# Kernel tuning notes

Hardware: AMD Instinct MI355X
Metric: run time of the kernel (lower is better)

Reference implementation:

```python
import jax, jax.numpy as jnp
import numpy as np

N = 50000   # nodes
E = 800000  # edges
C = 64      # node feature channels (0e)
A = 4       # edge attr channels
B = 16      # edge embedding (radial basis) size
H = 8       # radial MLP hidden size
D = 32      # query/key channels
P = 16      # node attr channels
R_MAX = 5.0


def setup_inputs() -> dict:
    key = jax.random.key(0)
    ks = jax.random.split(key, 20)
    w = lambda k, shape, fan_in: (jax.random.normal(k, shape, jnp.float32) / np.sqrt(fan_in).astype(np.float32))
    inp = {
        "node_feats": jax.random.normal(ks[0], (N, C), jnp.float32),
        "node_attrs": jax.random.normal(ks[1], (N, P), jnp.float32),
        "edge_embedding": jax.random.uniform(ks[2], (E, B), jnp.float32),
        "edge_attrs": jax.random.normal(ks[3], (E, A), jnp.float32),
        "positions": jax.random.normal(ks[4], (N, 3), jnp.float32) * 0.3,  # keep lengths < r_max
        "edge_src": jax.random.randint(ks[5], (E,), 0, N),
        "edge_dst": jax.random.randint(ks[6], (E,), 0, N),
        # parameters
        "W_q": w(ks[7], (C, D), C),            # h_q Linear
        "W1_k": w(ks[8], (B, H), B),           # radial MLP for tp_k
        "W2_k": w(ks[9], (H, C * A), H),
        "W1_v": w(ks[10], (B, H), B),          # radial MLP for tp_v
        "W2_v": w(ks[11], (H, C * A), H),
        "W_lin_k": w(ks[12], (C, D), C),       # linear_k
        "W_lin_v": w(ks[13], (C, C), C),       # linear_v
        "W_dot": w(ks[14], (D, D), D * D),     # FullyConnectedTensorProduct(q,k,'0e')
        "W_sc": w(ks[15], (C, P, C), C * P),   # self connection FCTP
    }
    return inp


def soft_unit_step(x):
    safe = jnp.where(x > 0, x, 1.0)
    return jnp.where(x > 0, jnp.exp(-1.0 / safe), 0.0)


def uvu_tp(x_src, edge_attrs, edge_embedding, W1, W2):
    # radial MLP -> per-edge, per-path weights [E, C, A]; 'uvu' tensor product on scalars
    wgt = (jax.nn.silu(edge_embedding @ W1) @ W2).reshape(-1, C, A)
    return x_src * (jnp.einsum('eca,ea->ec', wgt, edge_attrs) / np.sqrt(A).astype(np.float32))


def reference(node_feats, node_attrs, edge_embedding, edge_attrs, positions,
              edge_src, edge_dst, W_q, W1_k, W2_k, W1_v, W2_v,
              W_lin_k, W_lin_v, W_dot, W_sc):
    q = (node_feats @ W_q)[edge_dst]                              # [E, D]
    x_src = node_feats[edge_src]                                  # [E, C]
    k = uvu_tp(x_src, edge_attrs, edge_embedding, W1_k, W2_k) @ W_lin_k  # [E, D]
    v = uvu_tp(x_src, edge_attrs, edge_embedding, W1_v, W2_v) @ W_lin_v  # [E, C]

    edge_vec = positions[edge_dst] - positions[edge_src]
    edge_length = jnp.linalg.norm(edge_vec, axis=1)               # [E]
    cutoff = soft_unit_step(2.0 * R_MAX * (1.0 - edge_length / R_MAX))

    score = jnp.einsum('ei,ij,ej->e', q, W_dot, k)                # weighted bilinear dot -> 0e
    expv = cutoff * jnp.exp(score)                                # [E]
    z = jax.ops.segment_sum(expv, edge_dst, num_segments=N)       # softmax normalizer
    z = jnp.where(z == 0, 1.0, z)
    alpha = expv / z[edge_dst]
    msg = jnp.sqrt(jax.nn.relu(alpha))[:, None] * v               # [E, C]
    node_out = jax.ops.segment_sum(msg, edge_dst, num_segments=N)  # [N, C]

    sc = jnp.einsum('nc,np,cpo->no', node_feats, node_attrs, W_sc)
    return node_out + sc
```

## Files before the change

kernel.cpp:

```cpp
#include <hip/hip_runtime.h>
#include <math.h>

#define NN 50000
#define EE 800000
#define NPAD 50176

typedef __attribute__((ext_vector_type(8))) short short8v;
typedef __attribute__((ext_vector_type(4))) float f32x4;

static __device__ __forceinline__ short bf16r(float x) {
  union { float f; unsigned u; } v; v.f = x;
  unsigned r = v.u + 0x7FFFu + ((v.u >> 16) & 1u);
  return (short)(r >> 16);
}
static __device__ __forceinline__ float bf2f(unsigned u) {
  union { unsigned u; float f; } v; v.u = u << 16;
  return v.f;
}
static __device__ __forceinline__ unsigned pk2(float a, float b) {
  return (unsigned)(unsigned short)bf16r(a) | ((unsigned)(unsigned short)bf16r(b) << 16);
}


__global__ __launch_bounds__(256) void prep_kernel(
    const float* __restrict__ Wq, const float* __restrict__ Wdot,
    const float* __restrict__ Wlk, const float* __restrict__ W2k,
    const float* __restrict__ W2v, const float* __restrict__ Wlv,
    const float* __restrict__ Wsc, float* __restrict__ M,
    unsigned short* __restrict__ w2kT, unsigned short* __restrict__ w2vT,
    unsigned short* __restrict__ wlvb, unsigned short* __restrict__ wscb,
    int* __restrict__ cur)
{
  const int tid = threadIdx.x;
  const int b = blockIdx.x;
  if (b == 0) {
    __shared__ float tmp[2048];
#pragma unroll
    for (int r = 0; r < 8; ++r) {
      int idx = tid + r * 256;
      int cin = idx >> 5, d = idx & 31;
      float a = 0.f;
      for (int j = 0; j < 32; ++j) a = fmaf(Wq[cin * 32 + j], Wdot[j * 32 + d], a);
      tmp[idx] = a;
    }
    __syncthreads();
#pragma unroll
    for (int r = 0; r < 16; ++r) {
      int idx = tid + r * 256;
      int cin = idx >> 6, c = idx & 63;
      float a = 0.f;
      for (int d = 0; d < 32; ++d) a = fmaf(tmp[cin * 32 + d], Wlk[c * 32 + d], a);
      M[idx] = a;
    }
#pragma unroll
    for (int r = 0; r < 8; ++r) {
      int idx = tid + r * 256;
      int c = idx >> 5, k = idx & 31, h = k >> 2, a = k & 3;
      w2kT[idx] = (unsigned short)bf16r(W2k[h * 256 + c * 4 + a]);
      w2vT[idx] = (unsigned short)bf16r(W2v[h * 256 + c * 4 + a]);
    }
#pragma unroll
    for (int r = 0; r < 16; ++r) {
      int idx = tid + r * 256;
      int o = idx >> 6, c = idx & 63;
      wlvb[idx] = (unsigned short)bf16r(Wlv[c * 64 + o]);
    }
  } else if (b <= 196) {
    cur[(b - 1) * 256 + tid] = 0;
  } else {
    int w = (b - 197) * 256 + tid;
    int c = w & 63, o = (w >> 6) & 63, p = w >> 12;
    wscb[w] = (unsigned short)bf16r(Wsc[c * 1024 + p * 64 + o]);
  }
}

__global__ __launch_bounds__(256) void hist_zero(
    const int* __restrict__ edst, int* __restrict__ cur, float4* __restrict__ zu)
{
  int i = blockIdx.x * 256 + threadIdx.x;
  float4 zf = make_float4(0.f, 0.f, 0.f, 0.f);
  zu[i] = zf;
  if (i < 12544) zu[800000 + i] = zf;
  atomicAdd(&cur[edst[i]], 1);
}

__global__ __launch_bounds__(256) void scanA_kernel(
    int* __restrict__ cur, int* __restrict__ bsum)
{
  __shared__ int s[256];
  const int tid = threadIdx.x;
  const int i = blockIdx.x * 256 + tid;
  int v = cur[i];
  s[tid] = v;
  __syncthreads();
  for (int off = 1; off < 256; off <<= 1) {
    int t = (tid >= off) ? s[tid - off] : 0;
    __syncthreads();
    s[tid] += t;
    __syncthreads();
  }
  cur[i] = s[tid] - v;
  if (tid == 255) bsum[blockIdx.x] = s[255];
}

__global__ __launch_bounds__(256) void scanB_kernel(int* __restrict__ bsum)
{
  __shared__ int s[256];
  const int tid = threadIdx.x;
  int v = (tid < 196) ? bsum[tid] : 0;
  s[tid] = v;
  __syncthreads();
  for (int off = 1; off < 256; off <<= 1) {
    int t = (tid >= off) ? s[tid - off] : 0;
    __syncthreads();
    s[tid] += t;
    __syncthreads();
  }
  if (tid < 196) bsum[tid] = s[tid] - v;
}

__global__ __launch_bounds__(256) void scatter_fused(
    const int* __restrict__ esrc, const int* __restrict__ edst,
    const float* __restrict__ ea, const float* __restrict__ eb,
    const float* __restrict__ pos, const float* __restrict__ W1k,
    const float* __restrict__ W1v, int* __restrict__ cur,
    const int* __restrict__ bsum, int* __restrict__ perm,
    float* __restrict__ rec)
{
  int e = blockIdx.x * 256 + threadIdx.x;
  int s = esrc[e], d = edst[e];
  int r = atomicAdd(&cur[d], 1) + bsum[d >> 8];
  perm[r] = e;
  float dx = pos[d * 3 + 0] - pos[s * 3 + 0];
  float dy = pos[d * 3 + 1] - pos[s * 3 + 1];
  float dz = pos[d * 3 + 2] - pos[s * 3 + 2];
  float len = sqrtf(fmaf(dx, dx, fmaf(dy, dy, dz * dz)));
  float arg = 10.f - 2.f * len;
  float cl = (arg > 0.f) ? __expf(-1.f / arg) : 0.f;
  const f32x4* eb4 = reinterpret_cast<const f32x4*>(eb);
  f32x4 q0 = eb4[e * 4 + 0], q1 = eb4[e * 4 + 1],
        q2 = eb4[e * 4 + 2], q3 = eb4[e * 4 + 3];
  float ebv[16] = {q0.x, q0.y, q0.z, q0.w, q1.x, q1.y, q1.z, q1.w,
                   q2.x, q2.y, q2.z, q2.w, q3.x, q3.y, q3.z, q3.w};
  float h[16];
#pragma unroll
  for (int j = 0; j < 16; ++j) h[j] = 0.f;
#pragma unroll
  for (int b = 0; b < 16; ++b) {
    float x = ebv[b];
#pragma unroll
    for (int j = 0; j < 8; ++j) {
      h[j]     = fmaf(x, W1k[b * 8 + j], h[j]);
      h[8 + j] = fmaf(x, W1v[b * 8 + j], h[8 + j]);
    }
  }
#pragma unroll
  for (int j = 0; j < 16; ++j) h[j] = h[j] / (1.f + __expf(-h[j]));

  f32x4 a4 = reinterpret_cast<const f32x4*>(ea)[e];
  f32x4* rp4 = reinterpret_cast<f32x4*>(rec + (size_t)e * 12);
  f32x4 w0, w1, w2;
  w0.x = cl;
  w0.y = __uint_as_float(pk2(a4.x, a4.y));
  w0.z = __uint_as_float(pk2(a4.z, a4.w));
  w0.w = 0.f;
  w1.x = __uint_as_float(pk2(h[0], h[1]));
  w1.y = __uint_as_float(pk2(h[2], h[3]));
  w1.z = __uint_as_float(pk2(h[4], h[5]));
  w1.w = __uint_as_float(pk2(h[6], h[7]));
  w2.x = __uint_as_float(pk2(h[8], h[9]));
  w2.y = __uint_as_float(pk2(h[10], h[11]));
  w2.z = __uint_as_float(pk2(h[12], h[13]));
  w2.w = __uint_as_float(pk2(h[14], h[15]));
  rp4[0] = w0;
  rp4[1] = w1;
  rp4[2] = w2;
}

__global__ __launch_bounds__(256) void tq_kernel(
    const float* __restrict__ nf, const float* __restrict__ M,
    unsigned short* __restrict__ tqb, unsigned short* __restrict__ nfb)
{
  __shared__ float Ml[4096];
  __shared__ float nfl[64 * 68];
  const int tid = threadIdx.x;
  const int base = blockIdx.x * 64;
#pragma unroll
  for (int r = 0; r < 4; ++r) {
    int idx = tid + r * 256;
    reinterpret_cast<float4*>(Ml)[idx] = reinterpret_cast<const float4*>(M)[idx];
  }
#pragma unroll
  for (int r = 0; r < 4; ++r) {
    int idx = tid + r * 256;
    int row = idx >> 4, c4 = idx & 15;
    float4 v = make_float4(0.f, 0.f, 0.f, 0.f);
    if (base + row < NN) v = reinterpret_cast<const float4*>(nf)[(base + row) * 16 + c4];
    *reinterpret_cast<float4*>(&nfl[row * 68 + c4 * 4]) = v;
  }
  __syncthreads();
  const int to = tid & 15, tn = tid >> 4;
  float4 acc[4] = {make_float4(0,0,0,0), make_float4(0,0,0,0),
                   make_float4(0,0,0,0), make_float4(0,0,0,0)};
  for (int c = 0; c < 64; ++c) {
    float4 m = reinterpret_cast<const float4*>(Ml)[c * 16 + to];
#pragma unroll
    for (int i = 0; i < 4; ++i) {
      float x = nfl[(tn * 4 + i) * 68 + c];
      acc[i].x = fmaf(x, m.x, acc[i].x);
      acc[i].y = fmaf(x, m.y, acc[i].y);
      acc[i].z = fmaf(x, m.z, acc[i].z);
      acc[i].w = fmaf(x, m.w, acc[i].w);
    }
  }
#pragma unroll
  for (int i = 0; i < 4; ++i) {
    int n = base + tn * 4 + i;
    if (n < NN) {
      unsigned* tp = reinterpret_cast<unsigned*>(tqb) + (size_t)n * 32 + to * 2;
      tp[0] = pk2(acc[i].x, acc[i].y);
      tp[1] = pk2(acc[i].z, acc[i].w);
    }
  }
#pragma unroll
  for (int r = 0; r < 8; ++r) {
    int idx = tid + r * 256;
    int row = idx >> 5, cp = idx & 31;
    int n = base + row;
    if (n < NN) {
      reinterpret_cast<unsigned*>(nfb)[(size_t)n * 32 + cp] =
          pk2(nfl[row * 68 + cp * 2], nfl[row * 68 + cp * 2 + 1]);
    }
  }
}

__global__ __launch_bounds__(256) void edge_kernel(
    const unsigned short* __restrict__ nfb, const unsigned short* __restrict__ tqb,
    const float* __restrict__ rec, const int* __restrict__ perm,
    const int* __restrict__ esrc, const int* __restrict__ edst,
    const unsigned short* __restrict__ w2kT, const unsigned short* __restrict__ w2vT,
    float* __restrict__ z, float* __restrict__ U)
{
  __shared__ float xsAll[4][16 * 68];
  __shared__ int   esAll[4][16];
  __shared__ int   edAll[4][16];
  __shared__ float clAll[4][16];
  __shared__ float evAll[4][16];
  const int tid  = threadIdx.x;
  const int lane = tid & 63;
  const int w = tid >> 6;
  const int lo = lane & 15, hi = lane >> 4;
  const int sb = (blockIdx.x * 4 + w) * 16;
  float* xs = xsAll[w];
  int*   es = esAll[w];
  int*   ed = edAll[w];
  float* cl = clAll[w];
  float* evs = evAll[w];

  short8v bk[4], bv[4];
#pragma unroll
  for (int t = 0; t < 4; ++t) {
    bk[t] = *reinterpret_cast<const short8v*>(&w2kT[(16 * t + lo) * 32 + hi * 8]);
    bv[t] = *reinterpret_cast<const short8v*>(&w2vT[(16 * t + lo) * 32 + hi * 8]);
  }

  const int eL = perm[sb + lo];
  const unsigned* ru = reinterpret_cast<const unsigned*>(rec);
  const size_t rb = (size_t)eL * 12;
  unsigned ea01 = ru[rb + 1];
  unsigned ea23 = ru[rb + 2];
  unsigned k01  = ru[rb + 4 + hi];
  unsigned v01  = ru[rb + 8 + hi];
  if (hi == 0) {
    es[lo] = esrc[eL];
    ed[lo] = edst[eL];
    cl[lo] = rec[rb];
  }
  __builtin_amdgcn_wave_barrier();

#pragma unroll
  for (int r = 0; r < 2; ++r) {
    int idx = lane + r * 64;
    int e = idx >> 3, c8 = idx & 7;
    float4 pv = reinterpret_cast<const float4*>(nfb)[(size_t)es[e] * 8 + c8];
    unsigned u0 = __float_as_uint(pv.x), u1 = __float_as_uint(pv.y),
             u2 = __float_as_uint(pv.z), u3 = __float_as_uint(pv.w);
    float* xp = &xs[e * 68 + c8 * 8];
    xp[0] = bf2f(u0 & 0xffffu); xp[1] = bf2f(u0 >> 16);
    xp[2] = bf2f(u1 & 0xffffu); xp[3] = bf2f(u1 >> 16);
    xp[4] = bf2f(u2 & 0xffffu); xp[5] = bf2f(u2 >> 16);
    xp[6] = bf2f(u3 & 0xffffu); xp[7] = bf2f(u3 >> 16);
  }

  float ax = bf2f(ea01 & 0xffffu), ay = bf2f(ea01 >> 16);
  float az = bf2f(ea23 & 0xffffu), aw = bf2f(ea23 >> 16);
  float hk0 = bf2f(k01 & 0xffffu), hk1 = bf2f(k01 >> 16);
  float hv0 = bf2f(v01 & 0xffffu), hv1 = bf2f(v01 >> 16);
  short8v ak, av;
  ak[0] = bf16r(hk0 * ax); ak[1] = bf16r(hk0 * ay);
  ak[2] = bf16r(hk0 * az); ak[3] = bf16r(hk0 * aw);
  ak[4] = bf16r(hk1 * ax); ak[5] = bf16r(hk1 * ay);
  ak[6] = bf16r(hk1 * az); ak[7] = bf16r(hk1 * aw);
  av[0] = bf16r(hv0 * ax); av[1] = bf16r(hv0 * ay);
  av[2] = bf16r(hv0 * az); av[3] = bf16r(hv0 * aw);
  av[4] = bf16r(hv1 * ax); av[5] = bf16r(hv1 * ay);
  av[6] = bf16r(hv1 * az); av[7] = bf16r(hv1 * aw);
  __builtin_amdgcn_wave_barrier();

  f32x4 zero = {0.f, 0.f, 0.f, 0.f};
  f32x4 ack[4], acv[4];
#pragma unroll
  for (int t = 0; t < 4; ++t) {
    ack[t] = __builtin_amdgcn_mfma_f32_16x16x32_bf16(ak, bk[t], zero, 0, 0, 0);
    acv[t] = __builtin_amdgcn_mfma_f32_16x16x32_bf16(av, bv[t], zero, 0, 0, 0);
  }

  const int erow = 4 * hi;
  const unsigned short* tp0 = tqb + (size_t)ed[erow + 0] * 64;
  const unsigned short* tp1 = tqb + (size_t)ed[erow + 1] * 64;
  const unsigned short* tp2 = tqb + (size_t)ed[erow + 2] * 64;
  const unsigned short* tp3 = tqb + (size_t)ed[erow + 3] * 64;
  float p0 = 0.f, p1 = 0.f, p2 = 0.f, p3 = 0.f;
#pragma unroll
  for (int t = 0; t < 4; ++t) {
    int c = lo + 16 * t;
    p0 = fmaf(xs[(erow + 0) * 68 + c] * bf2f(tp0[c]), ack[t][0], p0);
    p1 = fmaf(xs[(erow + 1) * 68 + c] * bf2f(tp1[c]), ack[t][1], p1);
    p2 = fmaf(xs[(erow + 2) * 68 + c] * bf2f(tp2[c]), ack[t][2], p2);
    p3 = fmaf(xs[(erow + 3) * 68 + c] * bf2f(tp3[c]), ack[t][3], p3);
  }
#pragma unroll
  for (int off = 1; off < 16; off <<= 1) {
    p0 += __shfl_xor(p0, off);
    p1 += __shfl_xor(p1, off);
    p2 += __shfl_xor(p2, off);
    p3 += __shfl_xor(p3, off);
  }
  float ev0 = cl[erow + 0] * __expf(0.5f * p0);
  float ev1 = cl[erow + 1] * __expf(0.5f * p1);
  float ev2 = cl[erow + 2] * __expf(0.5f * p2);
  float ev3 = cl[erow + 3] * __expf(0.5f * p3);
  float se0 = sqrtf(ev0), se1 = sqrtf(ev1), se2 = sqrtf(ev2), se3 = sqrtf(ev3);
  if (lo < 4) {
    float ev = (lo == 0) ? ev0 : (lo == 1) ? ev1 : (lo == 2) ? ev2 : ev3;
    evs[erow + lo] = ev;
  }
#pragma unroll
  for (int i = 0; i < 4; ++i) {
    const float se = (i == 0) ? se0 : (i == 1) ? se1 : (i == 2) ? se2 : se3;
    float* xr = &xs[(erow + i) * 68 + lo];
#pragma unroll
    for (int t = 0; t < 4; ++t) {
      xr[16 * t] = se * xr[16 * t] * acv[t][i];
    }
  }
  __builtin_amdgcn_wave_barrier();
  {
    const int c = lane;
    float acc = 0.f, evacc = 0.f;
    int prev = ed[0];
#pragma unroll
    for (int r = 0; r < 16; ++r) {
      int d = ed[r];
      if (d != prev) {
        unsafeAtomicAdd(&U[prev * 64 + c], acc);
        if (c == 0) unsafeAtomicAdd(&z[prev], evacc);
        acc = 0.f; evacc = 0.f; prev = d;
      }
      acc += xs[r * 68 + c];
      if (c == 0) evacc += evs[r];
    }
    unsafeAtomicAdd(&U[prev * 64 + c], acc);
    if (c == 0) unsafeAtomicAdd(&z[prev], evacc);
  }
}

__global__ __launch_bounds__(256, 4) void final_kernel(
    const float* __restrict__ nf, const float* __restrict__ na,
    const float* __restrict__ U, const float* __restrict__ z,
    const unsigned short* __restrict__ wscb, const unsigned short* __restrict__ wlvb,
    float* __restrict__ out)
{
  __shared__ float nfl[64 * 68];
  __shared__ float Ul[64 * 68];
  __shared__ float nal[64 * 17];
  __shared__ float sl[64];
  const int tid = threadIdx.x;
  const int lane = tid & 63;
  const int lo = lane & 15, hi = lane >> 4;
  const int w = tid >> 6;
  const int nb = blockIdx.x * 64;

#pragma unroll
  for (int r = 0; r < 4; ++r) {
    int idx = tid + r * 256;
    int row = idx >> 4, c4 = idx & 15;
    int n = nb + row; if (n >= NN) n = NN - 1;
    float4 v = reinterpret_cast<const float4*>(nf)[n * 16 + c4];
    *reinterpret_cast<float4*>(&nfl[row * 68 + c4 * 4]) = v;
    float4 u = reinterpret_cast<const float4*>(U)[n * 16 + c4];
    *reinterpret_cast<float4*>(&Ul[row * 68 + c4 * 4]) = u;
  }
#pragma unroll
  for (int r = 0; r < 4; ++r) {
    int idx = tid + r * 256;
    int row = idx >> 4, p = idx & 15;
    int n = nb + row; if (n >= NN) n = NN - 1;
    nal[row * 17 + p] = na[n * 16 + p];
  }
  if (tid < 64) {
    int n = nb + tid; if (n >= NN) n = NN - 1;
    float zz = z[n];
    sl[tid] = (zz > 0.f) ? 0.5f * rsqrtf(zz) : 0.f;
  }
  __syncthreads();

  const int row = 16 * w + lo;
  short8v anf[2], au[2];
#pragma unroll
  for (int kk = 0; kk < 2; ++kk) {
#pragma unroll
    for (int j = 0; j < 8; ++j) {
      anf[kk][j] = bf16r(nfl[row * 68 + 32 * kk + 8 * hi + j]);
      au[kk][j]  = bf16r(Ul[row * 68 + 32 * kk + 8 * hi + j]);
    }
  }

  f32x4 zeroA = {0.f, 0.f, 0.f, 0.f};
  f32x4 accS[4] = {zeroA, zeroA, zeroA, zeroA};
  f32x4 accU[4] = {zeroA, zeroA, zeroA, zeroA};

#pragma unroll
  for (int t = 0; t < 4; ++t) {
    short8v b0 = *reinterpret_cast<const short8v*>(&wlvb[(16 * t + lo) * 64 + 8 * hi]);
    short8v b1 = *reinterpret_cast<const short8v*>(&wlvb[(16 * t + lo) * 64 + 32 + 8 * hi]);
    accU[t] = __builtin_amdgcn_mfma_f32_16x16x32_bf16(au[0], b0, accU[t], 0, 0, 0);
    accU[t] = __builtin_amdgcn_mfma_f32_16x16x32_bf16(au[1], b1, accU[t], 0, 0, 0);
  }
#pragma unroll 1
  for (int p = 0; p < 16; ++p) {
    f32x4 cp[4] = {zeroA, zeroA, zeroA, zeroA};
#pragma unroll
    for (int t = 0; t < 4; ++t) {
      const int bbase = (p * 64 + 16 * t + lo) * 64 + 8 * hi;
      short8v b0 = *reinterpret_cast<const short8v*>(&wscb[bbase]);
      short8v b1 = *reinterpret_cast<const short8v*>(&wscb[bbase + 32]);
      cp[t] = __builtin_amdgcn_mfma_f32_16x16x32_bf16(anf[0], b0, cp[t], 0, 0, 0);
      cp[t] = __builtin_amdgcn_mfma_f32_16x16x32_bf16(anf[1], b1, cp[t], 0, 0, 0);
    }
#pragma unroll
    for (int i = 0; i < 4; ++i) {
      float nav = nal[(16 * w + 4 * hi + i) * 17 + p];
#pragma unroll
      for (int t = 0; t < 4; ++t) accS[t][i] = fmaf(nav, cp[t][i], accS[t][i]);
    }
  }
#pragma unroll
  for (int i = 0; i < 4; ++i) {
    int n = nb + 16 * w + 4 * hi + i;
    if (n < NN) {
      float s = sl[16 * w + 4 * hi + i];
#pragma unroll
      for (int t = 0; t < 4; ++t) {
        out[n * 64 + 16 * t + lo] = fmaf(s, accU[t][i], accS[t][i]);
      }
    }
  }
}

extern "C" void kernel_launch(void* const* d_in, const int* in_sizes, int n_in,
                              void* d_out, int out_size, void* d_ws, size_t ws_size,
                              hipStream_t stream) {
  const float* nf   = (const float*)d_in[0];
  const float* na   = (const float*)d_in[1];
  const float* eb   = (const float*)d_in[2];
  const float* ea   = (const float*)d_in[3];
  const float* pos  = (const float*)d_in[4];
  const int*   esrc = (const int*)d_in[5];
  const int*   edst = (const int*)d_in[6];
  const float* Wq   = (const float*)d_in[7];
  const float* W1k  = (const float*)d_in[8];
  const float* W2k  = (const float*)d_in[9];
  const float* W1v  = (const float*)d_in[10];
  const float* W2v  = (const float*)d_in[11];
  const float* Wlk  = (const float*)d_in[12];
  const float* Wlv  = (const float*)d_in[13];
  const float* Wdot = (const float*)d_in[14];
  const float* Wsc  = (const float*)d_in[15];
  float* out = (float*)d_out;

  float* wsf = (float*)d_ws;
  float* z    = wsf;
  float* U    = wsf + 50176;
  unsigned short* nfb = (unsigned short*)(wsf + 3250176);
  unsigned short* tqb = (unsigned short*)(wsf + 4850176);
  unsigned short* w2kT = (unsigned short*)(wsf + 6450176);
  unsigned short* w2vT = (unsigned short*)(wsf + 6451200);
  unsigned short* wlvb = (unsigned short*)(wsf + 6452224);
  unsigned short* wscb = (unsigned short*)(wsf + 6454272);
  int*   cur  = (int*)(wsf + 6487040);
  int*   bsum = (int*)(wsf + 6537216);
  float* M    = wsf + 6537472;
  float* rec  = wsf + 6541568;
  int*   perm = (int*)(wsf + 16141568);

  prep_kernel<<<453, 256, 0, stream>>>(Wq, Wdot, Wlk, W2k, W2v, Wlv, Wsc,
                                       M, w2kT, w2vT, wlvb, wscb, cur);
  tq_kernel<<<(NN + 63) / 64, 256, 0, stream>>>(nf, M, tqb, nfb);
  hist_zero<<<EE / 256, 256, 0, stream>>>(edst, cur, (float4*)z);
  scanA_kernel<<<NPAD / 256, 256, 0, stream>>>(cur, bsum);
  scanB_kernel<<<1, 256, 0, stream>>>(bsum);
  scatter_fused<<<EE / 256, 256, 0, stream>>>(esrc, edst, ea, eb, pos, W1k, W1v,
                                              cur, bsum, perm, rec);
  edge_kernel<<<EE / 64, 256, 0, stream>>>(nfb, tqb, rec, perm, esrc, edst,
                                           w2kT, w2vT, z, U);
  final_kernel<<<(NN + 63) / 64, 256, 0, stream>>>(nf, na, U, z, wscb, wlvb, out);
}
```

Before: 305.2 us.

## Merge tq and histogram kernels, fuse two-level scan with last-block pattern

Combines the node projection kernel and the edge histogram/zeroing kernel into one launch by splitting the grid on block index. It also merges the two scan passes into a single kernel, where the last block to finish (tracked by an atomic counter in bsum[255], reset in prep) scans the block sums. The packed record layout is interleaved so each edge-kernel lane loads its k and v halves with one 8-byte load. The aim is to remove two launches and their gaps, and to let the two independent workloads overlap. In exchange it adds a threadfence and an atomic counter, and the fused kernel reserves the tq kernel's shared memory even for histogram blocks, which may reduce their occupancy.

```diff
diff --git a/kernel.cpp b/kernel.cpp
--- a/kernel.cpp
+++ b/kernel.cpp
@@ -29,7 +29,7 @@
     const float* __restrict__ Wsc, float* __restrict__ M,
     unsigned short* __restrict__ w2kT, unsigned short* __restrict__ w2vT,
     unsigned short* __restrict__ wlvb, unsigned short* __restrict__ wscb,
-    int* __restrict__ cur)
+    int* __restrict__ cur, int* __restrict__ bsum)
 {
   const int tid = threadIdx.x;
   const int b = blockIdx.x;
@@ -67,6 +67,7 @@
     }
   } else if (b <= 196) {
     cur[(b - 1) * 256 + tid] = 0;
+    if (b == 1 && tid == 0) bsum[255] = 0;
   } else {
     int w = (b - 197) * 256 + tid;
     int c = w & 63, o = (w >> 6) & 63, p = w >> 12;
@@ -74,20 +75,78 @@
   }
 }
 
-__global__ __launch_bounds__(256) void hist_zero(
-    const int* __restrict__ edst, int* __restrict__ cur, float4* __restrict__ zu)
+__global__ __launch_bounds__(256) void tqhist_kernel(
+    const float* __restrict__ nf, const float* __restrict__ M,
+    const int* __restrict__ edst, int* __restrict__ cur,
+    float4* __restrict__ zu,
+    unsigned short* __restrict__ tqb, unsigned short* __restrict__ nfb)
 {
-  int i = blockIdx.x * 256 + threadIdx.x;
-  float4 zf = make_float4(0.f, 0.f, 0.f, 0.f);
-  zu[i] = zf;
-  if (i < 12544) zu[800000 + i] = zf;
-  atomicAdd(&cur[edst[i]], 1);
-}
-
-__global__ __launch_bounds__(256) void scanA_kernel(
+  __shared__ float Ml[4096];
+  __shared__ float nfl[64 * 68];
+  const int tid = threadIdx.x;
+  if (blockIdx.x < 3125) {
+    int i = blockIdx.x * 256 + tid;
+    float4 zf = make_float4(0.f, 0.f, 0.f, 0.f);
+    zu[i] = zf;
+    if (i < 12544) zu[800000 + i] = zf;
+    atomicAdd(&cur[edst[i]], 1);
+    return;
+  }
+  const int base = (blockIdx.x - 3125) * 64;
+#pragma unroll
+  for (int r = 0; r < 4; ++r) {
+    int idx = tid + r * 256;
+    reinterpret_cast<float4*>(Ml)[idx] = reinterpret_cast<const float4*>(M)[idx];
+  }
+#pragma unroll
+  for (int r = 0; r < 4; ++r) {
+    int idx = tid + r * 256;
+    int row = idx >> 4, c4 = idx & 15;
+    float4 v = make_float4(0.f, 0.f, 0.f, 0.f);
+    if (base + row < NN) v = reinterpret_cast<const float4*>(nf)[(base + row) * 16 + c4];
+    *reinterpret_cast<float4*>(&nfl[row * 68 + c4 * 4]) = v;
+  }
+  __syncthreads();
+  const int to = tid & 15, tn = tid >> 4;
+  float4 acc[4] = {make_float4(0,0,0,0), make_float4(0,0,0,0),
+                   make_float4(0,0,0,0), make_float4(0,0,0,0)};
+  for (int c = 0; c < 64; ++c) {
+    float4 m = reinterpret_cast<const float4*>(Ml)[c * 16 + to];
+#pragma unroll
+    for (int i = 0; i < 4; ++i) {
+      float x = nfl[(tn * 4 + i) * 68 + c];
+      acc[i].x = fmaf(x, m.x, acc[i].x);
+      acc[i].y = fmaf(x, m.y, acc[i].y);
+      acc[i].z = fmaf(x, m.z, acc[i].z);
+      acc[i].w = fmaf(x, m.w, acc[i].w);
+    }
+  }
+#pragma unroll
+  for (int i = 0; i < 4; ++i) {
+    int n = base + tn * 4 + i;
+    if (n < NN) {
+      unsigned* tp = reinterpret_cast<unsigned*>(tqb) + (size_t)n * 32 + to * 2;
+      tp[0] = pk2(acc[i].x, acc[i].y);
+      tp[1] = pk2(acc[i].z, acc[i].w);
+    }
+  }
+#pragma unroll
+  for (int r = 0; r < 8; ++r) {
+    int idx = tid + r * 256;
+    int row = idx >> 5, cp = idx & 31;
+    int n = base + row;
+    if (n < NN) {
+      reinterpret_cast<unsigned*>(nfb)[(size_t)n * 32 + cp] =
+          pk2(nfl[row * 68 + cp * 2], nfl[row * 68 + cp * 2 + 1]);
+    }
+  }
+}
+
+__global__ __launch_bounds__(256) void scanAB_kernel(
     int* __restrict__ cur, int* __restrict__ bsum)
 {
   __shared__ int s[256];
+  __shared__ int isLast;
   const int tid = threadIdx.x;
   const int i = blockIdx.x * 256 + tid;
   int v = cur[i];
@@ -101,14 +160,12 @@
   }
   cur[i] = s[tid] - v;
   if (tid == 255) bsum[blockIdx.x] = s[255];
-}
-
-__global__ __launch_bounds__(256) void scanB_kernel(int* __restrict__ bsum)
-{
-  __shared__ int s[256];
-  const int tid = threadIdx.x;
-  int v = (tid < 196) ? bsum[tid] : 0;
-  s[tid] = v;
+  __threadfence();
+  if (tid == 0) isLast = (atomicAdd(&bsum[255], 1) == 195);
+  __syncthreads();
+  if (!isLast) return;
+  int v2 = (tid < 196) ? atomicAdd(&bsum[tid], 0) : 0;
+  s[tid] = v2;
   __syncthreads();
   for (int off = 1; off < 256; off <<= 1) {
     int t = (tid >= off) ? s[tid - off] : 0;
@@ -116,7 +173,7 @@
     s[tid] += t;
     __syncthreads();
   }
-  if (tid < 196) bsum[tid] = s[tid] - v;
+  if (tid < 196) bsum[tid] = s[tid] - v2;
 }
 
 __global__ __launch_bounds__(256) void scatter_fused(
@@ -165,73 +222,16 @@
   w0.z = __uint_as_float(pk2(a4.z, a4.w));
   w0.w = 0.f;
   w1.x = __uint_as_float(pk2(h[0], h[1]));
-  w1.y = __uint_as_float(pk2(h[2], h[3]));
-  w1.z = __uint_as_float(pk2(h[4], h[5]));
-  w1.w = __uint_as_float(pk2(h[6], h[7]));
-  w2.x = __uint_as_float(pk2(h[8], h[9]));
-  w2.y = __uint_as_float(pk2(h[10], h[11]));
-  w2.z = __uint_as_float(pk2(h[12], h[13]));
+  w1.y = __uint_as_float(pk2(h[8], h[9]));
+  w1.z = __uint_as_float(pk2(h[2], h[3]));
+  w1.w = __uint_as_float(pk2(h[10], h[11]));
+  w2.x = __uint_as_float(pk2(h[4], h[5]));
+  w2.y = __uint_as_float(pk2(h[12], h[13]));
+  w2.z = __uint_as_float(pk2(h[6], h[7]));
   w2.w = __uint_as_float(pk2(h[14], h[15]));
   rp4[0] = w0;
   rp4[1] = w1;
   rp4[2] = w2;
-}
-
-__global__ __launch_bounds__(256) void tq_kernel(
-    const float* __restrict__ nf, const float* __restrict__ M,
-    unsigned short* __restrict__ tqb, unsigned short* __restrict__ nfb)
-{
-  __shared__ float Ml[4096];
-  __shared__ float nfl[64 * 68];
-  const int tid = threadIdx.x;
-  const int base = blockIdx.x * 64;
-#pragma unroll
-  for (int r = 0; r < 4; ++r) {
-    int idx = tid + r * 256;
-    reinterpret_cast<float4*>(Ml)[idx] = reinterpret_cast<const float4*>(M)[idx];
-  }
-#pragma unroll
-  for (int r = 0; r < 4; ++r) {
-    int idx = tid + r * 256;
-    int row = idx >> 4, c4 = idx & 15;
-    float4 v = make_float4(0.f, 0.f, 0.f, 0.f);
-    if (base + row < NN) v = reinterpret_cast<const float4*>(nf)[(base + row) * 16 + c4];
-    *reinterpret_cast<float4*>(&nfl[row * 68 + c4 * 4]) = v;
-  }
-  __syncthreads();
-  const int to = tid & 15, tn = tid >> 4;
-  float4 acc[4] = {make_float4(0,0,0,0), make_float4(0,0,0,0),
-                   make_float4(0,0,0,0), make_float4(0,0,0,0)};
-  for (int c = 0; c < 64; ++c) {
-    float4 m = reinterpret_cast<const float4*>(Ml)[c * 16 + to];
-#pragma unroll
-    for (int i = 0; i < 4; ++i) {
-      float x = nfl[(tn * 4 + i) * 68 + c];
-      acc[i].x = fmaf(x, m.x, acc[i].x);
-      acc[i].y = fmaf(x, m.y, acc[i].y);
-      acc[i].z = fmaf(x, m.z, acc[i].z);
-      acc[i].w = fmaf(x, m.w, acc[i].w);
-    }
-  }
-#pragma unroll
-  for (int i = 0; i < 4; ++i) {
-    int n = base + tn * 4 + i;
-    if (n < NN) {
-      unsigned* tp = reinterpret_cast<unsigned*>(tqb) + (size_t)n * 32 + to * 2;
-      tp[0] = pk2(acc[i].x, acc[i].y);
-      tp[1] = pk2(acc[i].z, acc[i].w);
-    }
-  }
-#pragma unroll
-  for (int r = 0; r < 8; ++r) {
-    int idx = tid + r * 256;
-    int row = idx >> 5, cp = idx & 31;
-    int n = base + row;
-    if (n < NN) {
-      reinterpret_cast<unsigned*>(nfb)[(size_t)n * 32 + cp] =
-          pk2(nfl[row * 68 + cp * 2], nfl[row * 68 + cp * 2 + 1]);
-    }
-  }
 }
 
 __global__ __launch_bounds__(256) void edge_kernel(
@@ -269,8 +269,8 @@
   const size_t rb = (size_t)eL * 12;
   unsigned ea01 = ru[rb + 1];
   unsigned ea23 = ru[rb + 2];
-  unsigned k01  = ru[rb + 4 + hi];
-  unsigned v01  = ru[rb + 8 + hi];
+  uint2 kv = *reinterpret_cast<const uint2*>(&ru[rb + 4 + 2 * hi]);
+  unsigned k01 = kv.x, v01 = kv.y;
   if (hi == 0) {
     es[lo] = esrc[eL];
     ed[lo] = edst[eL];
@@ -505,11 +505,9 @@
   int*   perm = (int*)(wsf + 16141568);
 
   prep_kernel<<<453, 256, 0, stream>>>(Wq, Wdot, Wlk, W2k, W2v, Wlv, Wsc,
-                                       M, w2kT, w2vT, wlvb, wscb, cur);
-  tq_kernel<<<(NN + 63) / 64, 256, 0, stream>>>(nf, M, tqb, nfb);
-  hist_zero<<<EE / 256, 256, 0, stream>>>(edst, cur, (float4*)z);
-  scanA_kernel<<<NPAD / 256, 256, 0, stream>>>(cur, bsum);
-  scanB_kernel<<<1, 256, 0, stream>>>(bsum);
+                                       M, w2kT, w2vT, wlvb, wscb, cur, bsum);
+  tqhist_kernel<<<3907, 256, 0, stream>>>(nf, M, edst, cur, (float4*)z, tqb, nfb);
+  scanAB_kernel<<<196, 256, 0, stream>>>(cur, bsum);
   scatter_fused<<<EE / 256, 256, 0, stream>>>(esrc, edst, ea, eb, pos, W1k, W1v,
                                               cur, bsum, perm, rec);
   edge_kernel<<<EE / 64, 256, 0, stream>>>(nfb, tqb, rec, perm, esrc, edst,
```

Measured after the change: 314.4 us. +3.0%, slower.
